# Kernel optimization log

Hardware: AMD Instinct MI355X
Metric: run time of the kernel (lower is better)

Reference implementation:

```python
import jax, jax.numpy as jnp
import numpy as np

C_M, C_Z, C, H = 256, 128, 32, 8
N_SEQ, N_RES = 256, 256
EPS = 1e-5


def _layer_norm(x, w, b):
    mu = jnp.mean(x, axis=-1, keepdims=True)
    var = jnp.mean(jnp.square(x - mu), axis=-1, keepdims=True)
    return (x - mu) * jax.lax.rsqrt(var + EPS) * w + b


def setup_inputs() -> dict:
    key = jax.random.key(0)
    ks = jax.random.split(key, 10)
    s = lambda fan_in: 1.0 / np.sqrt(fan_in)
    return {
        "m": jax.random.normal(ks[0], (N_SEQ, N_RES, C_M), jnp.float32),
        "z": jax.random.normal(ks[1], (N_RES, N_RES, C_Z), jnp.float32),
        "ln_m_w": jnp.ones((C_M,), jnp.float32),
        "ln_m_b": jnp.zeros((C_M,), jnp.float32),
        "ln_z_w": jnp.ones((C_Z,), jnp.float32),
        "ln_z_b": jnp.zeros((C_Z,), jnp.float32),
        "w_z": jax.random.normal(ks[2], (C_Z, H), jnp.float32) * s(C_Z),
        "w_q": jax.random.normal(ks[3], (C_M, H * C), jnp.float32) * s(C_M),
        "w_k": jax.random.normal(ks[4], (C_M, H * C), jnp.float32) * s(C_M),
        "w_v": jax.random.normal(ks[5], (C_M, H * C), jnp.float32) * s(C_M),
        "w_g": jax.random.normal(ks[6], (C_M, H * C), jnp.float32) * s(C_M),
        "b_g": jnp.zeros((H * C,), jnp.float32),
        "w_o": jax.random.normal(ks[7], (H * C, C_M), jnp.float32) * s(H * C),
        "b_o": jnp.zeros((C_M,), jnp.float32),
    }


def reference(m, z, ln_m_w, ln_m_b, ln_z_w, ln_z_b, w_z, w_q, w_k, w_v, w_g, b_g, w_o, b_o):
    S, R = m.shape[0], m.shape[1]
    mn = _layer_norm(m, ln_m_w, ln_m_b)                      # (S, R, c_m)
    # pair bias: LN + Linear(c_z -> H), then movedim(-1, -3): (R, R, H) -> (H, R, R)
    bias = jnp.moveaxis(_layer_norm(z, ln_z_w, ln_z_b) @ w_z, -1, -3)

    q = (mn @ w_q).reshape(S, R, H, C)
    k = (mn @ w_k).reshape(S, R, H, C)
    v = (mn @ w_v).reshape(S, R, H, C)

    scale = 1.0 / np.sqrt(C)
    # attention over residue axis (attn_dim=-2); bias broadcast over N_seq
    logits = jnp.einsum("sqhd,skhd->shqk", q, k) * scale + bias[None]  # (S, H, R, R)
    attn = jax.nn.softmax(logits, axis=-1)
    o = jnp.einsum("shqk,skhd->sqhd", attn, v).reshape(S, R, H * C)

    g = jax.nn.sigmoid(mn @ w_g + b_g)                       # (S, R, H*c)
    return (g * o) @ w_o + b_o                               # (S, R, c_m)
```

## Files before the change

### kernel.cpp

```cpp
#include <hip/hip_runtime.h>
#include <hip/hip_bf16.h>

typedef __hip_bfloat16 bf16;
typedef __attribute__((ext_vector_type(8))) short short8;
typedef __attribute__((ext_vector_type(16))) float f32x16;

#define NS 256
#define NR 256
#define CM 256
#define CZ 128
#define NH 8
#define CH 32
#define LN_EPS 1e-5f
#define LOG2E 1.4426950408889634f
#define SCALE2 (0.17677669529663687f * 1.4426950408889634f)

__device__ __forceinline__ unsigned pk_bf16(float lo, float hi) {
  unsigned r;
  asm volatile("v_cvt_pk_bf16_f32 %0, %1, %2" : "=v"(r) : "v"(lo), "v"(hi));
  return r;
}

__device__ __forceinline__ short8 load8(const bf16* p) {
  return __builtin_bit_cast(short8, *(const uint4*)p);
}

__global__ __launch_bounds__(256) void pack_w_kernel(
    const float* __restrict__ wq, const float* __restrict__ wk,
    const float* __restrict__ wv, const float* __restrict__ wg,
    const float* __restrict__ wo, bf16* __restrict__ dst) {
  int mat = blockIdx.y;
  const float* src = mat == 0 ? wq : mat == 1 ? wk : mat == 2 ? wv
                   : mat == 3 ? wg : wo;
  int t = blockIdx.x * 256 + threadIdx.x;
  int n = t & 255;
  int hi = (t >> 8) & 1;
  int kc = t >> 9;
  int kbase = kc * 16 + hi * 8;
  bf16 tmp[8];
  #pragma unroll
  for (int j = 0; j < 8; ++j)
    tmp[j] = __float2bfloat16(src[(size_t)(kbase + j) * 256 + n]);
  *(uint4*)(dst + (size_t)mat * 65536 +
            ((size_t)(kc * 2 + hi) * 256 + n) * 8) = *(const uint4*)tmp;
}

__global__ __launch_bounds__(256) void ln_m_kernel(
    const float* __restrict__ m, const float* __restrict__ w,
    const float* __restrict__ b, bf16* __restrict__ mn) {
  int row = blockIdx.x * 4 + (threadIdx.x >> 6);
  int lane = threadIdx.x & 63;

  float4 x = ((const float4*)(m + (size_t)row * CM))[lane];
  float sum = x.x + x.y + x.z + x.w;
  #pragma unroll
  for (int off = 32; off; off >>= 1) sum += __shfl_xor(sum, off);
  float mu = sum * (1.0f / CM);

  float dx = x.x - mu, dy = x.y - mu, dz = x.z - mu, dw = x.w - mu;
  float ss = dx * dx + dy * dy + dz * dz + dw * dw;
  #pragma unroll
  for (int off = 32; off; off >>= 1) ss += __shfl_xor(ss, off);
  float rs = rsqrtf(ss * (1.0f / CM) + LN_EPS);

  float4 wv = ((const float4*)w)[lane];
  float4 bv = ((const float4*)b)[lane];
  unsigned p0 = pk_bf16(dx * rs * wv.x + bv.x, dy * rs * wv.y + bv.y);
  unsigned p1 = pk_bf16(dz * rs * wv.z + bv.z, dw * rs * wv.w + bv.w);
  uint2 u;
  u.x = p0;
  u.y = p1;
  *(uint2*)(mn + (size_t)row * CM + lane * 4) = u;
}

__global__ __launch_bounds__(128) void bias_kernel(
    const float* __restrict__ z, const float* __restrict__ w,
    const float* __restrict__ b, const float* __restrict__ wz,
    float* __restrict__ biasT) {
  int row = blockIdx.x;
  int t = threadIdx.x;
  __shared__ float red[2];
  __shared__ float zn[CZ];
  __shared__ float part[16][9];

  float x = z[(size_t)row * CZ + t];

  float v = x;
  #pragma unroll
  for (int off = 32; off; off >>= 1) v += __shfl_xor(v, off);
  if ((t & 63) == 0) red[t >> 6] = v;
  __syncthreads();
  float mu = (red[0] + red[1]) * (1.0f / CZ);
  float d = x - mu;
  __syncthreads();

  v = d * d;
  #pragma unroll
  for (int off = 32; off; off >>= 1) v += __shfl_xor(v, off);
  if ((t & 63) == 0) red[t >> 6] = v;
  __syncthreads();
  float var = (red[0] + red[1]) * (1.0f / CZ);

  zn[t] = d * rsqrtf(var + LN_EPS) * w[t] + b[t];
  __syncthreads();

  int h = t & 7, grp = t >> 3;
  float acc = 0.0f;
  #pragma unroll
  for (int cc = 0; cc < 8; ++cc) {
    int c = grp * 8 + cc;
    acc += zn[c] * wz[c * NH + h];
  }
  part[grp][h] = acc;
  __syncthreads();

  if (t < NH) {
    float s = 0.0f;
    #pragma unroll
    for (int g = 0; g < 16; ++g) s += part[g][t];
    int i = row >> 8, j = row & 255;
    biasT[(size_t)t * (NR * NR) + (size_t)j * NR + i] = s * LOG2E;
  }
}

__global__ __launch_bounds__(256, 2) void qkvg_mfma_kernel(
    const bf16* __restrict__ mn, const bf16* __restrict__ wp,
    const float* __restrict__ bg,
    bf16* __restrict__ qo, bf16* __restrict__ ko,
    bf16* __restrict__ vo, bf16* __restrict__ go) {
  int mat = threadIdx.x >> 6;
  int lane = threadIdx.x & 63;
  int lo = lane & 31, hi = lane >> 5;
  size_t m0 = (size_t)blockIdx.x * 32;

  const bf16* arow = mn + (m0 + lo) * 256 + hi * 8;
  const bf16* wbase = wp + (size_t)mat * 65536 + ((size_t)hi * 256 + lo) * 8;

  f32x16 acc[8] = {};
  #pragma unroll 2
  for (int kc = 0; kc < 16; ++kc) {
    short8 a = load8(arow + kc * 16);
    const bf16* wkc = wbase + (size_t)kc * 4096;
    #pragma unroll
    for (int nt = 0; nt < 8; ++nt) {
      short8 b = load8(wkc + nt * 256);
      acc[nt] = __builtin_amdgcn_mfma_f32_32x32x16_bf16(a, b, acc[nt], 0, 0, 0);
    }
  }

  bf16* outp = mat == 0 ? qo : mat == 1 ? ko : mat == 2 ? vo : go;
  if (mat == 3) {
    #pragma unroll
    for (int nt = 0; nt < 8; ++nt) {
      float bgv = bg[nt * 32 + lo];
      #pragma unroll
      for (int r = 0; r < 16; ++r) {
        int crow = (r & 3) + ((r >> 2) << 3) + (hi << 2);
        float sv = 1.0f / (1.0f + __expf(-(acc[nt][r] + bgv)));
        outp[(m0 + crow) * 256 + nt * 32 + lo] = __float2bfloat16(sv);
      }
    }
  } else {
    #pragma unroll
    for (int nt = 0; nt < 8; ++nt) {
      #pragma unroll
      for (int r = 0; r < 16; ++r) {
        int crow = (r & 3) + ((r >> 2) << 3) + (hi << 2);
        outp[(m0 + crow) * 256 + nt * 32 + lo] = __float2bfloat16(acc[nt][r]);
      }
    }
  }
}

__global__ __launch_bounds__(256) void transpose_v_kernel(
    const bf16* __restrict__ vo, bf16* __restrict__ vT) {
  int s = blockIdx.x >> 3, h = blockIdx.x & 7;
  int t = threadIdx.x;
  __shared__ bf16 tile[256][40];

  #pragma unroll
  for (int p = 0; p < 4; ++p) {
    int k = p * 64 + (t >> 2);
    int c0 = (t & 3) * 8;
    uint4 u = *(const uint4*)(vo + ((size_t)(s * 256 + k)) * 256 + h * 32 + c0);
    *(uint4*)&tile[k][c0] = u;
  }
  __syncthreads();

  int c = t >> 3, k0 = (t & 7) * 32;
  bf16 buf[32];
  #pragma unroll
  for (int j = 0; j < 32; ++j) buf[j] = tile[k0 + j][c];
  bf16* dst = vT + (((size_t)(s * 8 + h) * 32 + c) * 256 + k0);
  #pragma unroll
  for (int q = 0; q < 4; ++q)
    *(uint4*)(dst + q * 8) = *(const uint4*)(buf + q * 8);
}

__global__ __launch_bounds__(256, 2) void attn_mfma_kernel(
    const bf16* __restrict__ qb, const bf16* __restrict__ kb,
    const bf16* __restrict__ vT, const bf16* __restrict__ gb,
    const float* __restrict__ biasT, bf16* __restrict__ gob) {
  int wid = blockIdx.x * 4 + (threadIdx.x >> 6);
  int lane = threadIdx.x & 63;
  int lo = lane & 31;
  int hi = lane >> 5;
  int s = wid >> 6;
  int h = (wid >> 3) & 7;
  int q0 = (wid & 7) * 32;

  const size_t base = (size_t)s * NR * 256 + h * CH;

  short8 qf[2];
  #pragma unroll
  for (int cc = 0; cc < 2; ++cc)
    qf[cc] = load8(qb + base + (size_t)(q0 + lo) * 256 + cc * 16 + hi * 8);

  f32x16 acc[8];
  __builtin_amdgcn_s_setprio(1);
  #pragma unroll
  for (int t = 0; t < 8; ++t) {
    short8 kf0 = load8(kb + base + (size_t)(t * 32 + lo) * 256 + hi * 8);
    short8 kf1 = load8(kb + base + (size_t)(t * 32 + lo) * 256 + 16 + hi * 8);
    f32x16 z = {};
    acc[t] = __builtin_amdgcn_mfma_f32_32x32x16_bf16(kf0, qf[0], z, 0, 0, 0);
    acc[t] = __builtin_amdgcn_mfma_f32_32x32x16_bf16(kf1, qf[1], acc[t], 0, 0, 0);
  }
  __builtin_amdgcn_s_setprio(0);

  const float* bh = biasT + (size_t)h * (NR * NR) + q0 + lo;
  #pragma unroll
  for (int t = 0; t < 8; ++t) {
    #pragma unroll
    for (int r = 0; r < 16; ++r) {
      int kk = t * 32 + (r & 3) + ((r >> 2) << 3) + (hi << 2);
      acc[t][r] = fmaf(acc[t][r], SCALE2, bh[(size_t)kk * NR]);
    }
  }

  float mx = -3.0e38f;
  #pragma unroll
  for (int t = 0; t < 8; ++t)
    #pragma unroll
    for (int r = 0; r < 16; ++r) mx = fmaxf(mx, acc[t][r]);
  mx = fmaxf(mx, __shfl_xor(mx, 32));

  float l = 0.0f;
  #pragma unroll
  for (int t = 0; t < 8; ++t) {
    #pragma unroll
    for (int r = 0; r < 16; ++r) {
      float e = exp2f(acc[t][r] - mx);
      acc[t][r] = e;
      l += e;
    }
  }
  l += __shfl_xor(l, 32);

  f32x16 o = {};
  const bf16* vt = vT + ((size_t)(s * NH + h) * CH + lo) * 256;
  #pragma unroll
  for (int kc = 0; kc < 16; ++kc) {
    int t = kc >> 1;
    int rb = (kc & 1) << 3;
    unsigned uL0 = pk_bf16(acc[t][rb + 0], acc[t][rb + 1]);
    unsigned uL1 = pk_bf16(acc[t][rb + 2], acc[t][rb + 3]);
    unsigned uH0 = pk_bf16(acc[t][rb + 4], acc[t][rb + 5]);
    unsigned uH1 = pk_bf16(acc[t][rb + 6], acc[t][rb + 7]);
    unsigned sL0 = __shfl_xor(uL0, 32), sL1 = __shfl_xor(uL1, 32);
    unsigned sH0 = __shfl_xor(uH0, 32), sH1 = __shfl_xor(uH1, 32);
    uint4 pu;
    pu.x = hi ? sH0 : uL0;
    pu.y = hi ? sH1 : uL1;
    pu.z = hi ? uH0 : sL0;
    pu.w = hi ? uH1 : sL1;
    short8 pf = __builtin_bit_cast(short8, pu);
    short8 vf = load8(vt + kc * 16 + hi * 8);
    o = __builtin_amdgcn_mfma_f32_32x32x16_bf16(pf, vf, o, 0, 0, 0);
  }

  float linv = 1.0f / l;
  #pragma unroll
  for (int r = 0; r < 16; ++r) {
    int crow = (r & 3) + ((r >> 2) << 3) + (hi << 2);
    float li = __shfl(linv, crow);
    size_t idx = base + (size_t)(q0 + crow) * 256 + lo;
    float gg = __bfloat162float(gb[idx]);
    gob[idx] = __float2bfloat16(gg * o[r] * li);
  }
}

__global__ __launch_bounds__(256, 2) void out_mfma_kernel(
    const bf16* __restrict__ gob, const bf16* __restrict__ wop,
    const float* __restrict__ bo, float* __restrict__ out) {
  int wid = blockIdx.x * 4 + (threadIdx.x >> 6);
  int lane = threadIdx.x & 63;
  int lo = lane & 31, hi = lane >> 5;
  size_t m0 = (size_t)wid * 32;

  const bf16* arow = gob + (m0 + lo) * 256 + hi * 8;
  const bf16* wbase = wop + ((size_t)hi * 256 + lo) * 8;

  f32x16 acc[8] = {};
  #pragma unroll 2
  for (int kc = 0; kc < 16; ++kc) {
    short8 a = load8(arow + kc * 16);
    const bf16* wkc = wbase + (size_t)kc * 4096;
    #pragma unroll
    for (int nt = 0; nt < 8; ++nt) {
      short8 b = load8(wkc + nt * 256);
      acc[nt] = __builtin_amdgcn_mfma_f32_32x32x16_bf16(a, b, acc[nt], 0, 0, 0);
    }
  }

  #pragma unroll
  for (int nt = 0; nt < 8; ++nt) {
    float bv = bo[nt * 32 + lo];
    #pragma unroll
    for (int r = 0; r < 16; ++r) {
      int crow = (r & 3) + ((r >> 2) << 3) + (hi << 2);
      out[(m0 + crow) * 256 + nt * 32 + lo] = acc[nt][r] + bv;
    }
  }
}

extern "C" void kernel_launch(void* const* d_in, const int* in_sizes, int n_in,
                              void* d_out, int out_size, void* d_ws, size_t ws_size,
                              hipStream_t stream) {
  const float* m      = (const float*)d_in[0];
  const float* z      = (const float*)d_in[1];
  const float* ln_m_w = (const float*)d_in[2];
  const float* ln_m_b = (const float*)d_in[3];
  const float* ln_z_w = (const float*)d_in[4];
  const float* ln_z_b = (const float*)d_in[5];
  const float* w_z    = (const float*)d_in[6];
  const float* w_q    = (const float*)d_in[7];
  const float* w_k    = (const float*)d_in[8];
  const float* w_v    = (const float*)d_in[9];
  const float* w_g    = (const float*)d_in[10];
  const float* b_g    = (const float*)d_in[11];
  const float* w_o    = (const float*)d_in[12];
  const float* b_o    = (const float*)d_in[13];
  float* out = (float*)d_out;

  const size_t SZ = (size_t)NS * NR * 256;

  bf16* mn   = (bf16*)d_ws;
  bf16* qb   = mn + SZ;
  bf16* kb   = qb + SZ;
  bf16* vo   = kb + SZ;
  bf16* gb   = vo + SZ;
  bf16* gob  = gb + SZ;
  float* biasT = (float*)(gob + SZ);
  bf16* wp   = (bf16*)(biasT + NH * NR * NR);
  bf16* wop  = wp + 4 * 65536;
  bf16* vT   = mn;

  pack_w_kernel<<<dim3(32, 5), 256, 0, stream>>>(w_q, w_k, w_v, w_g, w_o, wp);
  ln_m_kernel<<<(NS * NR) / 4, 256, 0, stream>>>(m, ln_m_w, ln_m_b, mn);
  bias_kernel<<<NR * NR, 128, 0, stream>>>(z, ln_z_w, ln_z_b, w_z, biasT);
  qkvg_mfma_kernel<<<(NS * NR) / 32, 256, 0, stream>>>(mn, wp, b_g,
                                                       qb, kb, vo, gb);
  transpose_v_kernel<<<NS * NH, 256, 0, stream>>>(vo, vT);
  attn_mfma_kernel<<<(NS * NH * 8) / 4, 256, 0, stream>>>(qb, kb, vT, gb,
                                                          biasT, gob);
  out_mfma_kernel<<<(NS * NR) / 32 / 4, 256, 0, stream>>>(gob, wop, b_o, out);
}
```

Before: 314.7 us.

## Pre-permute pair bias into MFMA accumulator layout and fold Q scale into projection

The bias kernel now writes the pair bias directly in the per-lane MFMA accumulator order, so the attention kernel loads it with contiguous float4 reads and uses it as the initial accumulator of the QK^T MFMA. Before, it did strided scalar gathers followed by a separate fma pass. The softmax scale (times log2e) is folded into the Q projection epilogue. The max reduction is restructured as a tree. Rounding Q after scaling in bf16 slightly changes numerics.

```diff
diff --git a/kernel.cpp b/kernel.cpp
--- a/kernel.cpp
+++ b/kernel.cpp
@@ -76,7 +76,7 @@
 __global__ __launch_bounds__(128) void bias_kernel(
     const float* __restrict__ z, const float* __restrict__ w,
     const float* __restrict__ b, const float* __restrict__ wz,
-    float* __restrict__ biasT) {
+    float* __restrict__ biasP) {
   int row = blockIdx.x;
   int t = threadIdx.x;
   __shared__ float red[2];
@@ -119,7 +119,12 @@
     #pragma unroll
     for (int g = 0; g < 16; ++g) s += part[g][t];
     int i = row >> 8, j = row & 255;
-    biasT[(size_t)t * (NR * NR) + (size_t)j * NR + i] = s * LOG2E;
+    int qt = i >> 5, lo = i & 31;
+    int tt = j >> 5, rem = j & 31;
+    int hi2 = (rem >> 2) & 1;
+    int r = ((rem >> 3) << 2) | (rem & 3);
+    biasP[(((size_t)t * 8 + qt) * 64 + (hi2 * 32 + lo)) * 128 + tt * 16 + r] =
+        s * LOG2E;
   }
 }
 
@@ -161,12 +166,14 @@
       }
     }
   } else {
+    float sc = (mat == 0) ? SCALE2 : 1.0f;
     #pragma unroll
     for (int nt = 0; nt < 8; ++nt) {
       #pragma unroll
       for (int r = 0; r < 16; ++r) {
         int crow = (r & 3) + ((r >> 2) << 3) + (hi << 2);
-        outp[(m0 + crow) * 256 + nt * 32 + lo] = __float2bfloat16(acc[nt][r]);
+        outp[(m0 + crow) * 256 + nt * 32 + lo] =
+            __float2bfloat16(acc[nt][r] * sc);
       }
     }
   }
@@ -200,16 +207,20 @@
 __global__ __launch_bounds__(256, 2) void attn_mfma_kernel(
     const bf16* __restrict__ qb, const bf16* __restrict__ kb,
     const bf16* __restrict__ vT, const bf16* __restrict__ gb,
-    const float* __restrict__ biasT, bf16* __restrict__ gob) {
+    const float* __restrict__ biasP, bf16* __restrict__ gob) {
   int wid = blockIdx.x * 4 + (threadIdx.x >> 6);
   int lane = threadIdx.x & 63;
   int lo = lane & 31;
   int hi = lane >> 5;
   int s = wid >> 6;
   int h = (wid >> 3) & 7;
-  int q0 = (wid & 7) * 32;
+  int qt = wid & 7;
+  int q0 = qt * 32;
 
   const size_t base = (size_t)s * NR * 256 + h * CH;
+
+  const float4* bp =
+      (const float4*)(biasP + (((size_t)h * 8 + qt) * 64 + lane) * 128);
 
   short8 qf[2];
   #pragma unroll
@@ -222,27 +233,27 @@
   for (int t = 0; t < 8; ++t) {
     short8 kf0 = load8(kb + base + (size_t)(t * 32 + lo) * 256 + hi * 8);
     short8 kf1 = load8(kb + base + (size_t)(t * 32 + lo) * 256 + 16 + hi * 8);
-    f32x16 z = {};
-    acc[t] = __builtin_amdgcn_mfma_f32_32x32x16_bf16(kf0, qf[0], z, 0, 0, 0);
+    float4 b0 = bp[t * 4 + 0], b1 = bp[t * 4 + 1];
+    float4 b2 = bp[t * 4 + 2], b3 = bp[t * 4 + 3];
+    f32x16 c = {b0.x, b0.y, b0.z, b0.w, b1.x, b1.y, b1.z, b1.w,
+                b2.x, b2.y, b2.z, b2.w, b3.x, b3.y, b3.z, b3.w};
+    acc[t] = __builtin_amdgcn_mfma_f32_32x32x16_bf16(kf0, qf[0], c, 0, 0, 0);
     acc[t] = __builtin_amdgcn_mfma_f32_32x32x16_bf16(kf1, qf[1], acc[t], 0, 0, 0);
   }
   __builtin_amdgcn_s_setprio(0);
 
-  const float* bh = biasT + (size_t)h * (NR * NR) + q0 + lo;
+  float mx = -3.0e38f;
   #pragma unroll
   for (int t = 0; t < 8; ++t) {
-    #pragma unroll
-    for (int r = 0; r < 16; ++r) {
-      int kk = t * 32 + (r & 3) + ((r >> 2) << 3) + (hi << 2);
-      acc[t][r] = fmaf(acc[t][r], SCALE2, bh[(size_t)kk * NR]);
-    }
-  }
-
-  float mx = -3.0e38f;
-  #pragma unroll
-  for (int t = 0; t < 8; ++t)
-    #pragma unroll
-    for (int r = 0; r < 16; ++r) mx = fmaxf(mx, acc[t][r]);
+    float a = fmaxf(fmaxf(acc[t][0], acc[t][1]), acc[t][2]);
+    float b = fmaxf(fmaxf(acc[t][3], acc[t][4]), acc[t][5]);
+    float c = fmaxf(fmaxf(acc[t][6], acc[t][7]), acc[t][8]);
+    float d = fmaxf(fmaxf(acc[t][9], acc[t][10]), acc[t][11]);
+    float e = fmaxf(fmaxf(acc[t][12], acc[t][13]), acc[t][14]);
+    float g1 = fmaxf(fmaxf(a, b), c);
+    float g2 = fmaxf(fmaxf(d, e), acc[t][15]);
+    mx = fmaxf(fmaxf(g1, g2), mx);
+  }
   mx = fmaxf(mx, __shfl_xor(mx, 32));
 
   float l = 0.0f;
@@ -351,18 +362,18 @@
   bf16* vo   = kb + SZ;
   bf16* gb   = vo + SZ;
   bf16* gob  = gb + SZ;
-  float* biasT = (float*)(gob + SZ);
-  bf16* wp   = (bf16*)(biasT + NH * NR * NR);
+  float* biasP = (float*)(gob + SZ);
+  bf16* wp   = (bf16*)(biasP + NH * NR * NR);
   bf16* wop  = wp + 4 * 65536;
   bf16* vT   = mn;
 
   pack_w_kernel<<<dim3(32, 5), 256, 0, stream>>>(w_q, w_k, w_v, w_g, w_o, wp);
   ln_m_kernel<<<(NS * NR) / 4, 256, 0, stream>>>(m, ln_m_w, ln_m_b, mn);
-  bias_kernel<<<NR * NR, 128, 0, stream>>>(z, ln_z_w, ln_z_b, w_z, biasT);
+  bias_kernel<<<NR * NR, 128, 0, stream>>>(z, ln_z_w, ln_z_b, w_z, biasP);
   qkvg_mfma_kernel<<<(NS * NR) / 32, 256, 0, stream>>>(mn, wp, b_g,
                                                        qb, kb, vo, gb);
   transpose_v_kernel<<<NS * NH, 256, 0, stream>>>(vo, vT);
   attn_mfma_kernel<<<(NS * NH * 8) / 4, 256, 0, stream>>>(qb, kb, vT, gb,
-                                                          biasT, gob);
+                                                          biasP, gob);
   out_mfma_kernel<<<(NS * NR) / 32 / 4, 256, 0, stream>>>(gob, wop, b_o, out);
 }
```

New measurement: 352.0 us. 1.12x slower.
